# Optimization experiments

Hardware: AMD Instinct MI355X
Metric: run time of the kernel (lower is better)

Reference implementation:

```python
import jax, jax.numpy as jnp
import numpy as np

D = 512       # d_model
H = 8         # n_heads
HD = D // H   # head_dim
LYR = 4       # number_of_layers
PMT = 20      # pmt_len
L = 2048      # decode / target length (src_len - pmt_len)
BS = 1
DOUT = 3      # d_output (3 coding classes)
DFF = 4 * D
EPS = 1e-5


def layer_norm(x, g, b):
    m = jnp.mean(x, axis=-1, keepdims=True)
    v = jnp.mean((x - m) ** 2, axis=-1, keepdims=True)
    return (x - m) * jax.lax.rsqrt(v + EPS) * g + b


def rope(x):
    # x: (b, h, s, hd); half-split rotary with base 10000, positions = arange(s)
    half = x.shape[-1] // 2
    pos = jnp.arange(x.shape[2], dtype=jnp.float32)
    inv_freq = 1.0 / (10000.0 ** (jnp.arange(half, dtype=jnp.float32) / half))
    ang = pos[:, None] * inv_freq[None, :]          # (s, half)
    cos = jnp.cos(ang)[None, None]                  # (1,1,s,half)
    sin = jnp.sin(ang)[None, None]
    x1, x2 = x[..., :half], x[..., half:]
    return jnp.concatenate([x1 * cos - x2 * sin, x1 * sin + x2 * cos], axis=-1)


def mha(xq, xkv, wqkv, bqkv, wo, bo, key_mask, causal):
    # xq: (b, sq, D), xkv: (b, sk, D); key_mask: (b, sk) with 1=valid
    b, sq, _ = xq.shape
    sk = xkv.shape[1]
    q = xq @ wqkv[:, :D] + bqkv[:D]
    kv = xkv @ wqkv[:, D:] + bqkv[D:]
    k, v = kv[..., :D], kv[..., D:]
    q = q.reshape(b, sq, H, HD).transpose(0, 2, 1, 3)   # (b,h,sq,hd)
    k = k.reshape(b, sk, H, HD).transpose(0, 2, 1, 3)
    v = v.reshape(b, sk, H, HD).transpose(0, 2, 1, 3)
    q = rope(q)
    k = rope(k)
    scores = jnp.einsum('bhqd,bhkd->bhqk', q, k) / jnp.sqrt(jnp.float32(HD))
    scores = scores + jnp.where(key_mask[:, None, None, :] > 0, 0.0, -1e9)
    if causal:
        cm = jnp.tril(jnp.ones((sq, sk), dtype=bool))
        scores = jnp.where(cm[None, None], scores, -1e9)
    attn = jax.nn.softmax(scores, axis=-1)
    out = jnp.einsum('bhqk,bhkd->bhqd', attn, v)
    out = out.transpose(0, 2, 1, 3).reshape(b, sq, D)
    return out @ wo + bo


def setup_inputs() -> dict:
    key = jax.random.key(0)
    ks = jax.random.split(key, 16)
    s = 0.02
    p = lambda i, shape: jax.random.normal(ks[i], shape, jnp.float32) * s
    return {
        'trg_inputs': jax.random.normal(ks[0], (BS, L, DOUT), jnp.float32),
        'src_rep': jax.random.normal(ks[1], (BS, PMT + L, D), jnp.float32),
        'src_mask': jnp.ones((BS, L), jnp.float32),
        'emb_w': p(2, (DOUT, D)), 'emb_b': jnp.zeros((D,), jnp.float32),
        'sa_wqkv': p(3, (LYR, D, 3 * D)), 'sa_bqkv': jnp.zeros((LYR, 3 * D), jnp.float32),
        'sa_wo': p(4, (LYR, D, D)), 'sa_bo': jnp.zeros((LYR, D), jnp.float32),
        'ca_wqkv': p(5, (LYR, D, 3 * D)), 'ca_bqkv': jnp.zeros((LYR, 3 * D), jnp.float32),
        'ca_wo': p(6, (LYR, D, D)), 'ca_bo': jnp.zeros((LYR, D), jnp.float32),
        'ffn_w1': p(7, (LYR, D, DFF)), 'ffn_b1': jnp.zeros((LYR, DFF), jnp.float32),
        'ffn_w2': p(8, (LYR, DFF, D)), 'ffn_b2': jnp.zeros((LYR, D), jnp.float32),
        'ln_g': jnp.ones((LYR, 3, D), jnp.float32), 'ln_b': jnp.zeros((LYR, 3, D), jnp.float32),
        'lnf_g': jnp.ones((D,), jnp.float32), 'lnf_b': jnp.zeros((D,), jnp.float32),
        'gen_w': p(9, (D, DOUT)), 'gen_b': jnp.zeros((DOUT,), jnp.float32),
    }


def reference(trg_inputs, src_rep, src_mask, emb_w, emb_b, sa_wqkv, sa_bqkv, sa_wo, sa_bo,
              ca_wqkv, ca_bqkv, ca_wo, ca_bo, ffn_w1, ffn_b1, ffn_w2, ffn_b2,
              ln_g, ln_b, lnf_g, lnf_b, gen_w, gen_b):
    srb = src_rep[:, PMT:, :]                       # (bs, L, D)
    x = trg_inputs @ emb_w + emb_b                  # (bs, L, D)
    trg_mask = src_mask                             # parallel mode: trg_mask = src_mask
    for li in range(LYR):
        h = layer_norm(x, ln_g[li, 0], ln_b[li, 0])
        x = x + mha(h, h, sa_wqkv[li], sa_bqkv[li], sa_wo[li], sa_bo[li], trg_mask, causal=True)
        h = layer_norm(x, ln_g[li, 1], ln_b[li, 1])
        x = x + mha(h, srb, ca_wqkv[li], ca_bqkv[li], ca_wo[li], ca_bo[li], src_mask, causal=False)
        h = layer_norm(x, ln_g[li, 2], ln_b[li, 2])
        x = x + (jax.nn.relu(h @ ffn_w1[li] + ffn_b1[li]) @ ffn_w2[li] + ffn_b2[li])
    x = layer_norm(x, lnf_g, lnf_b)
    return x @ gen_w + gen_b                        # logits (bs, L, 3)
```

## Files before the change

kernel.cpp:

```cpp
#include <hip/hip_runtime.h>
#include <hip/hip_bf16.h>

#define SEQ 2048
#define DM 512
#define NHEAD 8
#define HDIM 64
#define DFFN 2048
#define PMTN 20

typedef __bf16 bf16x8 __attribute__((ext_vector_type(8)));
typedef float f32x4 __attribute__((ext_vector_type(4)));
typedef unsigned short u16x8 __attribute__((ext_vector_type(8)));

__device__ __forceinline__ float wave_sum(float v) {
#pragma unroll
  for (int off = 32; off; off >>= 1) v += __shfl_xor(v, off);
  return v;
}

__device__ __forceinline__ unsigned short f2b(float x) {
  __hip_bfloat16 h = __float2bfloat16(x);
  return *(unsigned short*)&h;
}

__device__ __forceinline__ void gll16(const __hip_bfloat16* g, __hip_bfloat16* l) {
  __builtin_amdgcn_global_load_lds(
      (const __attribute__((address_space(1))) unsigned int*)(g),
      (__attribute__((address_space(3))) unsigned int*)(l), 16, 0, 0);
}

__global__ __launch_bounds__(256) void prologue_kernel(
    const float* __restrict__ trg, const float* __restrict__ emb_w,
    const float* __restrict__ emb_b, float* __restrict__ X,
    const float* __restrict__ srb, __hip_bfloat16* __restrict__ SRBb,
    float2* __restrict__ rt, const float* __restrict__ mask,
    float* __restrict__ mb, int* __restrict__ mtflag) {
  const int b = blockIdx.x, t = threadIdx.x;
  if (b < 4096) {
    int idx = b * 256 + t;
    int r = idx >> 9, c = idx & 511;
    float t0 = trg[r * 3 + 0], t1 = trg[r * 3 + 1], t2 = trg[r * 3 + 2];
    X[idx] = t0 * emb_w[c] + t1 * emb_w[512 + c] + t2 * emb_w[1024 + c] + emb_b[c];
  } else if (b < 8192) {
    int i = (b - 4096) * 256 + t;
    SRBb[i] = __float2bfloat16(srb[i]);
  } else if (b < 8448) {
    int idx = (b - 8192) * 256 + t;
    int row = idx >> 5, i = idx & 31;
    float inv = __expf(-(float)i * (9.210340371976184f / 32.f));
    float sn, cs;
    sincosf((float)row * inv, &sn, &cs);
    rt[idx] = make_float2(cs, sn);
  } else {
    int i = (b - 8448) * 256 + t;
    bool masked = !(mask[i] > 0.f);
    mb[i] = masked ? -8.0e9f : 0.f;
    unsigned long long any = __ballot(masked);
    if ((t & 63) == 0) mtflag[i >> 6] = (any != 0ull) ? 1 : 0;
  }
}

__global__ __launch_bounds__(256) void ln_bf16_kernel(
    const float* __restrict__ x, const float* __restrict__ g,
    const float* __restrict__ b, __hip_bfloat16* __restrict__ o) {
  int row = blockIdx.x * 4 + (threadIdx.x >> 6);
  int lane = threadIdx.x & 63;
  const float* xr = x + (long)row * DM;
  float v[8];
  float s = 0.f;
#pragma unroll
  for (int j = 0; j < 8; j++) { v[j] = xr[lane + 64 * j]; s += v[j]; }
  s = wave_sum(s);
  float mean = s * (1.f / DM);
  float q = 0.f;
#pragma unroll
  for (int j = 0; j < 8; j++) { float d = v[j] - mean; q += d * d; }
  q = wave_sum(q);
  float r = rsqrtf(q * (1.f / DM) + 1e-5f);
  __hip_bfloat16* orow = o + (long)row * DM;
#pragma unroll
  for (int j = 0; j < 8; j++) {
    int c = lane + 64 * j;
    orow[c] = __float2bfloat16((v[j] - mean) * r * g[c] + b[c]);
  }
}

__global__ __launch_bounds__(256) void ln_gen_kernel(
    const float* __restrict__ x, const float* __restrict__ g,
    const float* __restrict__ b, const float* __restrict__ gw,
    const float* __restrict__ gb, float* __restrict__ out) {
  int row = blockIdx.x * 4 + (threadIdx.x >> 6);
  int lane = threadIdx.x & 63;
  const float* xr = x + (long)row * DM;
  float v[8];
  float s = 0.f;
#pragma unroll
  for (int j = 0; j < 8; j++) { v[j] = xr[lane + 64 * j]; s += v[j]; }
  s = wave_sum(s);
  float mean = s * (1.f / DM);
  float q = 0.f;
#pragma unroll
  for (int j = 0; j < 8; j++) { float d = v[j] - mean; q += d * d; }
  q = wave_sum(q);
  float r = rsqrtf(q * (1.f / DM) + 1e-5f);
  float a0 = 0.f, a1 = 0.f, a2 = 0.f;
#pragma unroll
  for (int j = 0; j < 8; j++) {
    int c = lane + 64 * j;
    float nv = (v[j] - mean) * r * g[c] + b[c];
    a0 = fmaf(nv, gw[c * 3 + 0], a0);
    a1 = fmaf(nv, gw[c * 3 + 1], a1);
    a2 = fmaf(nv, gw[c * 3 + 2], a2);
  }
  a0 = wave_sum(a0);
  a1 = wave_sum(a1);
  a2 = wave_sum(a2);
  if (lane == 0) {
    out[row * 3 + 0] = a0 + gb[0];
    out[row * 3 + 1] = a1 + gb[1];
    out[row * 3 + 2] = a2 + gb[2];
  }
}

__global__ __launch_bounds__(256) void transpose_layer_kernel(
    const float* __restrict__ wqkv, const float* __restrict__ wo,
    const float* __restrict__ cwqkv, const float* __restrict__ cwo,
    const float* __restrict__ w1, const float* __restrict__ w2,
    __hip_bfloat16* __restrict__ Wt) {
  int b = blockIdx.x;
  const float* W;
  __hip_bfloat16* O;
  int Kd, Nd;
  if (b < 192)      { W = wqkv;  O = Wt + 0;       Kd = 512;  Nd = 1536; }
  else if (b < 256) { W = wo;    O = Wt + 786432;  Kd = 512;  Nd = 512;  b -= 192; }
  else if (b < 448) { W = cwqkv; O = Wt + 1048576; Kd = 512;  Nd = 1536; b -= 256; }
  else if (b < 512) { W = cwo;   O = Wt + 1835008; Kd = 512;  Nd = 512;  b -= 448; }
  else if (b < 768) { W = w1;    O = Wt + 2097152; Kd = 512;  Nd = 2048; b -= 512; }
  else              { W = w2;    O = Wt + 3145728; Kd = 2048; Nd = 512;  b -= 768; }
  int tn = Nd >> 6;
  int k0 = (b / tn) * 64, n0 = (b % tn) * 64;
  __shared__ float T[64][65];
  int t = threadIdx.x;
  int rr = t >> 4, c4 = (t & 15) * 4;
#pragma unroll
  for (int p = 0; p < 4; p++) {
    int row = rr + p * 16;
    float4 v = *(const float4*)(W + (long)(k0 + row) * Nd + n0 + c4);
    T[row][c4 + 0] = v.x; T[row][c4 + 1] = v.y;
    T[row][c4 + 2] = v.z; T[row][c4 + 3] = v.w;
  }
  __syncthreads();
#pragma unroll
  for (int p = 0; p < 4; p++) {
    int row = rr + p * 16;
    ushort4 pk;
    pk.x = f2b(T[c4 + 0][row]); pk.y = f2b(T[c4 + 1][row]);
    pk.z = f2b(T[c4 + 2][row]); pk.w = f2b(T[c4 + 3][row]);
    *(ushort4*)(O + (long)(n0 + row) * Kd + k0 + c4) = pk;
  }
}

__global__ __launch_bounds__(256) void gemm_bf16_64(
    const __hip_bfloat16* __restrict__ A, int lda,
    const __hip_bfloat16* __restrict__ A2,
    const __hip_bfloat16* __restrict__ Bt, int ldb,
    const float* __restrict__ bias,
    const float* __restrict__ residual,
    float* __restrict__ Cf, __hip_bfloat16* __restrict__ Cb, int ldc,
    int K, int relu, int mode, const float2* __restrict__ rt,
    __hip_bfloat16* __restrict__ Qp, __hip_bfloat16* __restrict__ Kp,
    __hip_bfloat16* __restrict__ Vtp) {
  __shared__ __attribute__((aligned(16))) __hip_bfloat16 As[2][4096];
  __shared__ __attribute__((aligned(16))) __hip_bfloat16 Bs[2][4096];
  const int t = threadIdx.x;
  const int bx = blockIdx.x;
  const int nrow = bx * 64, m0 = blockIdx.y * 64;
  const int ptype = (mode == 0) ? 3 : (nrow < 512 ? 0 : (nrow < 1024 ? 1 : 2));
  const int head = (nrow >> 6) & 7;
  const __hip_bfloat16* Ause = (mode == 2 && bx >= 8) ? A2 : A;

  const int w = t >> 6, lane = t & 63;
  const int wr = w >> 1, wc = w & 1;
  const int fr = lane & 15, fk = lane >> 4;
  const int r0 = t & 63, c0 = t >> 6;
  const __hip_bfloat16* Arow = Ause + (long)(m0 + r0) * lda;
  const __hip_bfloat16* Brow = Bt + (long)(nrow + r0) * ldb;

  uint4 ra0 = *(const uint4*)(Arow + c0 * 8);
  uint4 ra1 = *(const uint4*)(Arow + (c0 + 4) * 8);
  uint4 rb0 = *(const uint4*)(Brow + c0 * 8);
  uint4 rb1 = *(const uint4*)(Brow + (c0 + 4) * 8);
  *(uint4*)(&As[0][(c0 * 64 + r0) * 8]) = ra0;
  *(uint4*)(&As[0][((c0 + 4) * 64 + r0) * 8]) = ra1;
  *(uint4*)(&Bs[0][(c0 * 64 + r0) * 8]) = rb0;
  *(uint4*)(&Bs[0][((c0 + 4) * 64 + r0) * 8]) = rb1;
  __syncthreads();

  f32x4 acc[2][2] = {};
  const int NK = K >> 6;
  for (int ks = 0; ks < NK; ++ks) {
    const int cur = ks & 1;
    if (ks + 1 < NK) {
      const int ko = (ks + 1) << 6;
      ra0 = *(const uint4*)(Arow + ko + c0 * 8);
      ra1 = *(const uint4*)(Arow + ko + (c0 + 4) * 8);
      rb0 = *(const uint4*)(Brow + ko + c0 * 8);
      rb1 = *(const uint4*)(Brow + ko + (c0 + 4) * 8);
    }
#pragma unroll
    for (int kk = 0; kk < 2; ++kk) {
      const int kc = kk * 4 + fk;
      bf16x8 a0 = *(const bf16x8*)(&As[cur][(kc * 64 + wr * 32 + fr) * 8]);
      bf16x8 a1 = *(const bf16x8*)(&As[cur][(kc * 64 + wr * 32 + 16 + fr) * 8]);
      bf16x8 b0 = *(const bf16x8*)(&Bs[cur][(kc * 64 + wc * 32 + fr) * 8]);
      bf16x8 b1 = *(const bf16x8*)(&Bs[cur][(kc * 64 + wc * 32 + 16 + fr) * 8]);
      acc[0][0] = __builtin_amdgcn_mfma_f32_16x16x32_bf16(a0, b0, acc[0][0], 0, 0, 0);
      acc[0][1] = __builtin_amdgcn_mfma_f32_16x16x32_bf16(a0, b1, acc[0][1], 0, 0, 0);
      acc[1][0] = __builtin_amdgcn_mfma_f32_16x16x32_bf16(a1, b0, acc[1][0], 0, 0, 0);
      acc[1][1] = __builtin_amdgcn_mfma_f32_16x16x32_bf16(a1, b1, acc[1][1], 0, 0, 0);
    }
    if (ks + 1 < NK) {
      const int nxt = cur ^ 1;
      *(uint4*)(&As[nxt][(c0 * 64 + r0) * 8]) = ra0;
      *(uint4*)(&As[nxt][((c0 + 4) * 64 + r0) * 8]) = ra1;
      *(uint4*)(&Bs[nxt][(c0 * 64 + r0) * 8]) = rb0;
      *(uint4*)(&Bs[nxt][((c0 + 4) * 64 + r0) * 8]) = rb1;
    }
    __syncthreads();
  }

  if (ptype == 3) {
#pragma unroll
    for (int m = 0; m < 2; ++m)
#pragma unroll
      for (int n = 0; n < 2; ++n)
#pragma unroll
        for (int j = 0; j < 4; ++j) {
          int r = m0 + wr * 32 + m * 16 + fk * 4 + j;
          int c = nrow + wc * 32 + n * 16 + fr;
          float v = acc[m][n][j] + bias[c];
          if (relu) v = fmaxf(v, 0.f);
          if (residual) v += residual[(long)r * ldc + c];
          if (Cf) Cf[(long)r * ldc + c] = v;
          if (Cb) Cb[(long)r * ldc + c] = __float2bfloat16(v);
        }
    return;
  }

  float* Lt = (float*)As;
#pragma unroll
  for (int m = 0; m < 2; ++m)
#pragma unroll
    for (int n = 0; n < 2; ++n)
#pragma unroll
      for (int j = 0; j < 4; ++j) {
        int rl = wr * 32 + m * 16 + fk * 4 + j;
        int cl = wc * 32 + n * 16 + fr;
        Lt[rl * 64 + (cl ^ (rl & 31))] = acc[m][n][j] + bias[nrow + cl];
      }
  __syncthreads();

  if (ptype == 2) {
    const int d = t >> 2, sc = (t & 3) * 16;
    u16x8 o0, o1;
#pragma unroll
    for (int s = 0; s < 8; s++) {
      o0[s] = f2b(Lt[(sc + s) * 64 + (d ^ ((sc + s) & 31))]);
      o1[s] = f2b(Lt[(sc + 8 + s) * 64 + (d ^ ((sc + 8 + s) & 31))]);
    }
    __hip_bfloat16* dst = Vtp + ((long)(head * 64 + d)) * SEQ + m0 + sc;
    *(u16x8*)dst = o0;
    *(u16x8*)(dst + 8) = o1;
  } else {
    const int r = t >> 2, i0 = (t & 3) * 8;
    const float2* rp = rt + (long)(m0 + r) * 32 + i0;
    u16x8 lo, hi;
#pragma unroll
    for (int p = 0; p < 8; p++) {
      float a = Lt[r * 64 + ((i0 + p) ^ (r & 31))];
      float b = Lt[r * 64 + ((i0 + p + 32) ^ (r & 31))];
      float2 cs = rp[p];
      lo[p] = f2b(a * cs.x - b * cs.y);
      hi[p] = f2b(a * cs.y + b * cs.x);
    }
    __hip_bfloat16* dst =
        (ptype == 0 ? Qp : Kp) + ((long)head * SEQ + m0 + r) * 64 + i0;
    *(u16x8*)dst = lo;
    *(u16x8*)(dst + 32) = hi;
  }
}

__global__ __launch_bounds__(256) void attn_part_kernel(
    const __hip_bfloat16* __restrict__ Qp, const __hip_bfloat16* __restrict__ Kp,
    const __hip_bfloat16* __restrict__ Vtp, const float* __restrict__ mbias,
    const int* __restrict__ mtflag,
    __hip_bfloat16* __restrict__ Op, float* __restrict__ Ml,
    int causal, int csz) {
  const int qt = blockIdx.x, ch = blockIdx.y, head = blockIdx.z;
  const int kv0 = ch * csz;
  if (causal && kv0 > qt * 64 + 63) return;
  const int kvlen = causal ? min(csz, qt * 64 + 64 - kv0) : csz;
  const int nt = (kvlen + 63) >> 6;

  __shared__ __attribute__((aligned(16))) __hip_bfloat16 Ks[2][4096];
  __shared__ __attribute__((aligned(16))) __hip_bfloat16 Vs[2][4096];
  __shared__ __attribute__((aligned(16))) __hip_bfloat16 Ps[4096];
  const int t = threadIdx.x, w = t >> 6, lane = t & 63;
  const int fr = lane & 15, fk = lane >> 4;
  const int qr = qt * 64 + w * 16 + fr;
  const int wq0 = qt * 64 + w * 16;
  const float SCL = 0.18033688011112042f;

  bf16x8 qa0, qa1;
  {
    const __hip_bfloat16* qp = Qp + ((long)head * SEQ + qr) * 64 + fk * 8;
    qa0 = *(const bf16x8*)qp;
    qa1 = *(const bf16x8*)(qp + 32);
  }
  const __hip_bfloat16* Kh = Kp + (long)head * SEQ * 64;
  const __hip_bfloat16* Vh = Vtp + (long)head * 64 * SEQ;
  const int skr = t & 63, skc = t >> 6;

  float m_i = -3e38f, l_i = 0.f;
  f32x4 o_[4] = {};
  const int sw2 = (fr & 7) << 4;

  {
    const __hip_bfloat16* ksrc = Kh + (long)(kv0 + skr) * 64 + skc * 8;
    gll16(ksrc, Ks[0] + t * 8);
    gll16(ksrc + 32, Ks[0] + t * 8 + 2048);
    const __hip_bfloat16* vsrc = Vh + (long)skr * SEQ + kv0 + skc * 8;
    gll16(vsrc, Vs[0] + t * 8);
    gll16(vsrc + 32, Vs[0] + t * 8 + 2048);
  }

  for (int tile = 0; tile < nt; ++tile) {
    __syncthreads();
    const int cur = tile & 1;
    if (tile + 1 < nt) {
      const int kb1 = kv0 + (tile + 1) * 64;
      const int nxt = cur ^ 1;
      const __hip_bfloat16* ksrc = Kh + (long)(kb1 + skr) * 64 + skc * 8;
      gll16(ksrc, Ks[nxt] + t * 8);
      gll16(ksrc + 32, Ks[nxt] + t * 8 + 2048);
      const __hip_bfloat16* vsrc = Vh + (long)skr * SEQ + kb1 + skc * 8;
      gll16(vsrc, Vs[nxt] + t * 8);
      gll16(vsrc + 32, Vs[nxt] + t * 8 + 2048);
    }
    const int kb = kv0 + tile * 64;
    const bool need = !causal || (kb <= wq0 + 15);
    if (need) {
      const bool diag = causal && (kb + 63 > wq0);
      const bool hasmask = mtflag[kb >> 6] != 0;

      f32x4 sacc[4];
      __builtin_amdgcn_s_setprio(1);
#pragma unroll
      for (int n = 0; n < 4; n++) {
        bf16x8 ka0 = *(const bf16x8*)(Ks[cur] + fk * 512 + (n * 16 + fr) * 8);
        bf16x8 ka1 = *(const bf16x8*)(Ks[cur] + (4 + fk) * 512 + (n * 16 + fr) * 8);
        f32x4 zz = {};
        zz = __builtin_amdgcn_mfma_f32_16x16x32_bf16(ka0, qa0, zz, 0, 0, 0);
        sacc[n] = __builtin_amdgcn_mfma_f32_16x16x32_bf16(ka1, qa1, zz, 0, 0, 0);
      }
      __builtin_amdgcn_s_setprio(0);

      float sv[4][4];
      float rm = -3e38f;
#pragma unroll
      for (int n = 0; n < 4; n++) {
        const int ka = kb + n * 16 + fk * 4;
        if (hasmask) {
          float4 mb = *(const float4*)(mbias + ka);
          sv[n][0] = sacc[n][0] + mb.x;
          sv[n][1] = sacc[n][1] + mb.y;
          sv[n][2] = sacc[n][2] + mb.z;
          sv[n][3] = sacc[n][3] + mb.w;
        } else {
          sv[n][0] = sacc[n][0]; sv[n][1] = sacc[n][1];
          sv[n][2] = sacc[n][2]; sv[n][3] = sacc[n][3];
        }
        if (diag) {
#pragma unroll
          for (int j = 0; j < 4; j++)
            if (ka + j > qr) sv[n][j] = -3e38f;
        }
#pragma unroll
        for (int j = 0; j < 4; j++) rm = fmaxf(rm, sv[n][j]);
      }
      rm = fmaxf(rm, __shfl_xor(rm, 16));
      rm = fmaxf(rm, __shfl_xor(rm, 32));
      if (!__all(rm <= m_i)) {
        float nm = fmaxf(m_i, rm);
        float f = exp2f((m_i - nm) * SCL);
        l_i *= f;
#pragma unroll
        for (int n = 0; n < 4; n++) o_[n] *= f;
        m_i = nm;
      }
#pragma unroll
      for (int n = 0; n < 4; n++) {
        float p0 = exp2f((sv[n][0] - m_i) * SCL);
        float p1 = exp2f((sv[n][1] - m_i) * SCL);
        float p2 = exp2f((sv[n][2] - m_i) * SCL);
        float p3 = exp2f((sv[n][3] - m_i) * SCL);
        l_i += (p0 + p1) + (p2 + p3);
        ushort4 pk4;
        pk4.x = f2b(p0); pk4.y = f2b(p1); pk4.z = f2b(p2); pk4.w = f2b(p3);
        *(ushort4*)((char*)Ps + ((w * 2048 + fr * 128 + (n * 16 + fk * 4) * 2) ^ sw2)) = pk4;
      }

      __builtin_amdgcn_s_setprio(1);
#pragma unroll
      for (int s = 0; s < 2; s++) {
        bf16x8 pb = *(const bf16x8*)((char*)Ps + ((w * 2048 + fr * 128 + s * 64 + fk * 16) ^ sw2));
#pragma unroll
        for (int n = 0; n < 4; n++) {
          bf16x8 va = *(const bf16x8*)(Vs[cur] + (s * 4 + fk) * 512 + (n * 16 + fr) * 8);
          o_[n] = __builtin_amdgcn_mfma_f32_16x16x32_bf16(va, pb, o_[n], 0, 0, 0);
        }
      }
      __builtin_amdgcn_s_setprio(0);
    }
  }

  l_i += __shfl_xor(l_i, 16);
  l_i += __shfl_xor(l_i, 32);

  const long bid = ((long)head * 32 + qt) * gridDim.y + ch;
  __hip_bfloat16* Ob = Op + bid * 4096;
#pragma unroll
  for (int n = 0; n < 4; n++) {
    ushort4 ov;
    ov.x = f2b(o_[n][0]); ov.y = f2b(o_[n][1]);
    ov.z = f2b(o_[n][2]); ov.w = f2b(o_[n][3]);
    *(ushort4*)(Ob + (w * 16 + fr) * 64 + n * 16 + fk * 4) = ov;
  }
  if (fk == 0) {
    float2 ml = make_float2(m_i, l_i);
    *(float2*)(Ml + bid * 128 + (w * 16 + fr) * 2) = ml;
  }
}

__global__ __launch_bounds__(256) void attn_combine_kernel(
    const __hip_bfloat16* __restrict__ Op, const float* __restrict__ Ml,
    __hip_bfloat16* __restrict__ O, int ldo, int causal, int csz, int nch) {
  const int qt = blockIdx.x, head = blockIdx.y;
  const int nc = causal ? min(nch, (qt * 64 + 63) / csz + 1) : nch;
  const int t = threadIdx.x;
  const int row = t >> 2, c16 = (t & 3) * 16;
  const long bid0 = ((long)head * 32 + qt) * nch;
  const float SCL = 0.18033688011112042f;
  float M = -3e38f;
  for (int c = 0; c < nc; c++) M = fmaxf(M, Ml[(bid0 + c) * 128 + row * 2]);
  float L = 0.f;
  float acc[16] = {};
  for (int c = 0; c < nc; c++) {
    float2 ml = *(const float2*)(Ml + (bid0 + c) * 128 + row * 2);
    float wg = exp2f((ml.x - M) * SCL);
    L += wg * ml.y;
    const __hip_bfloat16* base = Op + (bid0 + c) * 4096 + row * 64 + c16;
    bf16x8 a = *(const bf16x8*)base;
    bf16x8 b = *(const bf16x8*)(base + 8);
#pragma unroll
    for (int e = 0; e < 8; e++) {
      acc[e] += wg * (float)a[e];
      acc[8 + e] += wg * (float)b[e];
    }
  }
  float invL = 1.f / fmaxf(L, 1e-20f);
  u16x8 o0, o1;
#pragma unroll
  for (int e = 0; e < 8; e++) {
    o0[e] = f2b(acc[e] * invL);
    o1[e] = f2b(acc[8 + e] * invL);
  }
  __hip_bfloat16* orow = O + (long)(qt * 64 + row) * ldo + head * 64 + c16;
  *(u16x8*)orow = o0;
  *(u16x8*)(orow + 8) = o1;
}

extern "C" void kernel_launch(void* const* d_in, const int* in_sizes, int n_in,
                              void* d_out, int out_size, void* d_ws, size_t ws_size,
                              hipStream_t stream) {
  const float* trg      = (const float*)d_in[0];
  const float* src_rep  = (const float*)d_in[1];
  const float* src_mask = (const float*)d_in[2];
  const float* emb_w    = (const float*)d_in[3];
  const float* emb_b    = (const float*)d_in[4];
  const float* sa_wqkv  = (const float*)d_in[5];
  const float* sa_bqkv  = (const float*)d_in[6];
  const float* sa_wo    = (const float*)d_in[7];
  const float* sa_bo    = (const float*)d_in[8];
  const float* ca_wqkv  = (const float*)d_in[9];
  const float* ca_bqkv  = (const float*)d_in[10];
  const float* ca_wo    = (const float*)d_in[11];
  const float* ca_bo    = (const float*)d_in[12];
  const float* ffn_w1   = (const float*)d_in[13];
  const float* ffn_b1   = (const float*)d_in[14];
  const float* ffn_w2   = (const float*)d_in[15];
  const float* ffn_b2   = (const float*)d_in[16];
  const float* ln_g     = (const float*)d_in[17];
  const float* ln_b     = (const float*)d_in[18];
  const float* lnf_g    = (const float*)d_in[19];
  const float* lnf_b    = (const float*)d_in[20];
  const float* gen_w    = (const float*)d_in[21];
  const float* gen_b    = (const float*)d_in[22];

  const float* srb = src_rep + (long)PMTN * DM;

  char* wsb = (char*)d_ws;
  float*          X    = (float*)wsb;
  __hip_bfloat16* Hb   = (__hip_bfloat16*)(wsb + (4ul << 20));
  __hip_bfloat16* MID  = (__hip_bfloat16*)(wsb + (6ul << 20));
  __hip_bfloat16* Op   = MID;
  __hip_bfloat16* AO   = (__hip_bfloat16*)(wsb + (14ul << 20));
  __hip_bfloat16* SRBb = (__hip_bfloat16*)(wsb + (16ul << 20));
  float2*         rt   = (float2*)(wsb + (18ul << 20));
  float*          mbias= (float*)(wsb + (18ul << 20) + 524288);
  int*            mtfl = (int*)(wsb + (18ul << 20) + 532480);
  float*          Ml   = (float*)(wsb + (19ul << 20));
  __hip_bfloat16* Qp   = (__hip_bfloat16*)(wsb + (20ul << 20));
  __hip_bfloat16* Kp   = (__hip_bfloat16*)(wsb + (22ul << 20));
  __hip_bfloat16* Vtp  = (__hip_bfloat16*)(wsb + (24ul << 20));
  __hip_bfloat16* Wt   = (__hip_bfloat16*)(wsb + (26ul << 20));

  const int nch = 4;
  const int csz = SEQ / nch;

  prologue_kernel<<<8456, 256, 0, stream>>>(trg, emb_w, emb_b, X, srb, SRBb,
                                            rt, src_mask, mbias, mtfl);

  __hip_bfloat16* wqkvT  = Wt + 0;
  __hip_bfloat16* woT    = Wt + 786432;
  __hip_bfloat16* cwqkvT = Wt + 1048576;
  __hip_bfloat16* cwoT   = Wt + 1835008;
  __hip_bfloat16* w1T    = Wt + 2097152;
  __hip_bfloat16* w2T    = Wt + 3145728;

  for (int li = 0; li < 4; li++) {
    transpose_layer_kernel<<<1024, 256, 0, stream>>>(
        sa_wqkv + (long)li * DM * 3 * DM, sa_wo + (long)li * DM * DM,
        ca_wqkv + (long)li * DM * 3 * DM, ca_wo + (long)li * DM * DM,
        ffn_w1 + (long)li * DM * DFFN, ffn_w2 + (long)li * DFFN * DM, Wt);

    const float* bqkv  = sa_bqkv + (long)li * 3 * DM;
    const float* bo    = sa_bo + (long)li * DM;
    const float* cbqkv = ca_bqkv + (long)li * 3 * DM;
    const float* cbo   = ca_bo + (long)li * DM;
    const float* b1    = ffn_b1 + (long)li * DFFN;
    const float* b2    = ffn_b2 + (long)li * DM;
    const float* g0  = ln_g + (long)(li * 3 + 0) * DM;
    const float* bb0 = ln_b + (long)(li * 3 + 0) * DM;
    const float* g1  = ln_g + (long)(li * 3 + 1) * DM;
    const float* bb1 = ln_b + (long)(li * 3 + 1) * DM;
    const float* g2  = ln_g + (long)(li * 3 + 2) * DM;
    const float* bb2 = ln_b + (long)(li * 3 + 2) * DM;

    ln_bf16_kernel<<<512, 256, 0, stream>>>(X, g0, bb0, Hb);
    gemm_bf16_64<<<dim3(24, 32), 256, 0, stream>>>(
        Hb, DM, nullptr, wqkvT, DM, bqkv, nullptr, nullptr, nullptr, DM,
        DM, 0, 1, rt, Qp, Kp, Vtp);
    attn_part_kernel<<<dim3(32, nch, 8), 256, 0, stream>>>(
        Qp, Kp, Vtp, mbias, mtfl, Op, Ml, 1, csz);
    attn_combine_kernel<<<dim3(32, 8), 256, 0, stream>>>(
        Op, Ml, AO, DM, 1, csz, nch);
    gemm_bf16_64<<<dim3(8, 32), 256, 0, stream>>>(
        AO, DM, nullptr, woT, DM, bo, X, X, nullptr, DM,
        DM, 0, 0, nullptr, nullptr, nullptr, nullptr);

    ln_bf16_kernel<<<512, 256, 0, stream>>>(X, g1, bb1, Hb);
    gemm_bf16_64<<<dim3(24, 32), 256, 0, stream>>>(
        Hb, DM, SRBb, cwqkvT, DM, cbqkv, nullptr, nullptr, nullptr, DM,
        DM, 0, 2, rt, Qp, Kp, Vtp);
    attn_part_kernel<<<dim3(32, nch, 8), 256, 0, stream>>>(
        Qp, Kp, Vtp, mbias, mtfl, Op, Ml, 0, csz);
    attn_combine_kernel<<<dim3(32, 8), 256, 0, stream>>>(
        Op, Ml, AO, DM, 0, csz, nch);
    gemm_bf16_64<<<dim3(8, 32), 256, 0, stream>>>(
        AO, DM, nullptr, cwoT, DM, cbo, X, X, nullptr, DM,
        DM, 0, 0, nullptr, nullptr, nullptr, nullptr);

    ln_bf16_kernel<<<512, 256, 0, stream>>>(X, g2, bb2, Hb);
    gemm_bf16_64<<<dim3(32, 32), 256, 0, stream>>>(
        Hb, DM, nullptr, w1T, DM, b1, nullptr, nullptr, MID, DFFN,
        DM, 1, 0, nullptr, nullptr, nullptr, nullptr);
    gemm_bf16_64<<<dim3(8, 32), 256, 0, stream>>>(
        MID, DFFN, nullptr, w2T, DFFN, b2, X, X, nullptr, DM,
        DFFN, 0, 0, nullptr, nullptr, nullptr, nullptr);
  }

  ln_gen_kernel<<<512, 256, 0, stream>>>(X, lnf_g, lnf_b, gen_w, gen_b,
                                         (float*)d_out);
}
```

Before: 751.6 us.

## Fold softmax scale into Q projection and stage V through registers

Multiplies Q by the softmax log2 scale inside the projection epilogue, so the attention and combine kernels drop their per-element multiply before exp2. The mask bias shrinks to -1e9 to stay sensible in the rescaled domain. V tiles are now loaded into registers and written into a single LDS buffer each iteration instead of going through a double-buffered async global-to-LDS copy. This frees LDS but adds an extra barrier per tile and exposes V load latency more directly.

Measured after the change: 750.8 us. No clear change (-0.1%).

```diff
diff --git a/kernel.cpp b/kernel.cpp
--- a/kernel.cpp
+++ b/kernel.cpp
@@ -54,7 +54,7 @@
   } else {
     int i = (b - 8448) * 256 + t;
     bool masked = !(mask[i] > 0.f);
-    mb[i] = masked ? -8.0e9f : 0.f;
+    mb[i] = masked ? -1.0e9f : 0.f;
     unsigned long long any = __ballot(masked);
     if ((t & 63) == 0) mtflag[i >> 6] = (any != 0ull) ? 1 : 0;
   }
@@ -272,6 +272,7 @@
     *(u16x8*)dst = o0;
     *(u16x8*)(dst + 8) = o1;
   } else {
+    const float QS = (ptype == 0) ? 0.18033688011112042f : 1.0f;
     const int r = t >> 2, i0 = (t & 3) * 8;
     const float2* rp = rt + (long)(m0 + r) * 32 + i0;
     u16x8 lo, hi;
@@ -280,8 +281,8 @@
       float a = Lt[r * 64 + ((i0 + p) ^ (r & 31))];
       float b = Lt[r * 64 + ((i0 + p + 32) ^ (r & 31))];
       float2 cs = rp[p];
-      lo[p] = f2b(a * cs.x - b * cs.y);
-      hi[p] = f2b(a * cs.y + b * cs.x);
+      lo[p] = f2b((a * cs.x - b * cs.y) * QS);
+      hi[p] = f2b((a * cs.y + b * cs.x) * QS);
     }
     __hip_bfloat16* dst =
         (ptype == 0 ? Qp : Kp) + ((long)head * SEQ + m0 + r) * 64 + i0;
@@ -303,13 +304,12 @@
   const int nt = (kvlen + 63) >> 6;
 
   __shared__ __attribute__((aligned(16))) __hip_bfloat16 Ks[2][4096];
-  __shared__ __attribute__((aligned(16))) __hip_bfloat16 Vs[2][4096];
+  __shared__ __attribute__((aligned(16))) __hip_bfloat16 Vs[4096];
   __shared__ __attribute__((aligned(16))) __hip_bfloat16 Ps[4096];
   const int t = threadIdx.x, w = t >> 6, lane = t & 63;
   const int fr = lane & 15, fk = lane >> 4;
   const int qr = qt * 64 + w * 16 + fr;
   const int wq0 = qt * 64 + w * 16;
-  const float SCL = 0.18033688011112042f;
 
   bf16x8 qa0, qa1;
   {
@@ -325,18 +325,22 @@
   f32x4 o_[4] = {};
   const int sw2 = (fr & 7) << 4;
 
+  uint4 vr0, vr1;
   {
     const __hip_bfloat16* ksrc = Kh + (long)(kv0 + skr) * 64 + skc * 8;
     gll16(ksrc, Ks[0] + t * 8);
     gll16(ksrc + 32, Ks[0] + t * 8 + 2048);
     const __hip_bfloat16* vsrc = Vh + (long)skr * SEQ + kv0 + skc * 8;
-    gll16(vsrc, Vs[0] + t * 8);
-    gll16(vsrc + 32, Vs[0] + t * 8 + 2048);
+    vr0 = *(const uint4*)vsrc;
+    vr1 = *(const uint4*)(vsrc + 32);
   }
 
   for (int tile = 0; tile < nt; ++tile) {
+    const int cur = tile & 1;
     __syncthreads();
-    const int cur = tile & 1;
+    *(uint4*)(Vs + t * 8) = vr0;
+    *(uint4*)(Vs + t * 8 + 2048) = vr1;
+    __syncthreads();
     if (tile + 1 < nt) {
       const int kb1 = kv0 + (tile + 1) * 64;
       const int nxt = cur ^ 1;
@@ -344,8 +348,8 @@
       gll16(ksrc, Ks[nxt] + t * 8);
       gll16(ksrc + 32, Ks[nxt] + t * 8 + 2048);
       const __hip_bfloat16* vsrc = Vh + (long)skr * SEQ + kb1 + skc * 8;
-      gll16(vsrc, Vs[nxt] + t * 8);
-      gll16(vsrc + 32, Vs[nxt] + t * 8 + 2048);
+      vr0 = *(const uint4*)vsrc;
+      vr1 = *(const uint4*)(vsrc + 32);
     }
     const int kb = kv0 + tile * 64;
     const bool need = !causal || (kb <= wq0 + 15);
@@ -392,7 +396,7 @@
       rm = fmaxf(rm, __shfl_xor(rm, 32));
       if (!__all(rm <= m_i)) {
         float nm = fmaxf(m_i, rm);
-        float f = exp2f((m_i - nm) * SCL);
+        float f = exp2f(m_i - nm);
         l_i *= f;
 #pragma unroll
         for (int n = 0; n < 4; n++) o_[n] *= f;
@@ -400,10 +404,10 @@
       }
 #pragma unroll
       for (int n = 0; n < 4; n++) {
-        float p0 = exp2f((sv[n][0] - m_i) * SCL);
-        float p1 = exp2f((sv[n][1] - m_i) * SCL);
-        float p2 = exp2f((sv[n][2] - m_i) * SCL);
-        float p3 = exp2f((sv[n][3] - m_i) * SCL);
+        float p0 = exp2f(sv[n][0] - m_i);
+        float p1 = exp2f(sv[n][1] - m_i);
+        float p2 = exp2f(sv[n][2] - m_i);
+        float p3 = exp2f(sv[n][3] - m_i);
         l_i += (p0 + p1) + (p2 + p3);
         ushort4 pk4;
         pk4.x = f2b(p0); pk4.y = f2b(p1); pk4.z = f2b(p2); pk4.w = f2b(p3);
@@ -416,7 +420,7 @@
         bf16x8 pb = *(const bf16x8*)((char*)Ps + ((w * 2048 + fr * 128 + s * 64 + fk * 16) ^ sw2));
 #pragma unroll
         for (int n = 0; n < 4; n++) {
-          bf16x8 va = *(const bf16x8*)(Vs[cur] + (s * 4 + fk) * 512 + (n * 16 + fr) * 8);
+          bf16x8 va = *(const bf16x8*)(Vs + (s * 4 + fk) * 512 + (n * 16 + fr) * 8);
           o_[n] = __builtin_amdgcn_mfma_f32_16x16x32_bf16(va, pb, o_[n], 0, 0, 0);
         }
       }
@@ -450,14 +454,13 @@
   const int t = threadIdx.x;
   const int row = t >> 2, c16 = (t & 3) * 16;
   const long bid0 = ((long)head * 32 + qt) * nch;
-  const float SCL = 0.18033688011112042f;
   float M = -3e38f;
   for (int c = 0; c < nc; c++) M = fmaxf(M, Ml[(bid0 + c) * 128 + row * 2]);
   float L = 0.f;
   float acc[16] = {};
   for (int c = 0; c < nc; c++) {
     float2 ml = *(const float2*)(Ml + (bid0 + c) * 128 + row * 2);
-    float wg = exp2f((ml.x - M) * SCL);
+    float wg = exp2f(ml.x - M);
     L += wg * ml.y;
     const __hip_bfloat16* base = Op + (bid0 + c) * 4096 + row * 64 + c16;
     bf16x8 a = *(const bf16x8*)base;
```
